# Performance work log

Hardware: AMD Instinct MI355X
Metric: run time of the kernel (lower is better)

The kernel has to match this reference:

```python
import jax, jax.numpy as jnp
import numpy as np

EPS = 1e-5


def gcn_conv(x, edge_index, W, b):
    # PyG GCNConv: h = x @ W; add self-loops; symmetric deg^-1/2 normalization; scatter-add to dst; + bias
    n = x.shape[0]
    h = x @ W  # [N, out]
    loops = jnp.arange(n, dtype=edge_index.dtype)
    src = jnp.concatenate([edge_index[0], loops])
    dst = jnp.concatenate([edge_index[1], loops])
    deg = jax.ops.segment_sum(jnp.ones(src.shape[0], dtype=h.dtype), dst, num_segments=n)
    dinv = jnp.where(deg > 0, jax.lax.rsqrt(jnp.maximum(deg, 1e-12)), 0.0)
    norm = dinv[src] * dinv[dst]  # [E+N]
    out = jax.ops.segment_sum(h[src] * norm[:, None], dst, num_segments=n)
    return out + b


def setup_inputs() -> dict:
    key = jax.random.key(0)
    ks = jax.random.split(key, 10)
    N, E = 50000, 800000
    IN, HID, OUT = 128, 128, 64
    x = jax.random.normal(ks[0], (N, IN), dtype=jnp.float32)
    edge_index1 = jax.random.randint(ks[1], (2, E), 0, N, dtype=jnp.int64)
    edge_index2 = jax.random.randint(ks[2], (2, E), 0, N, dtype=jnp.int64)
    s1 = 1.0 / np.sqrt(IN)
    s2 = 1.0 / np.sqrt(HID)
    W1 = jax.random.uniform(ks[3], (IN, HID), jnp.float32, -s1, s1)
    b1 = jax.random.uniform(ks[4], (HID,), jnp.float32, -s1, s1)
    gamma = jnp.ones((HID,), jnp.float32)
    beta = jnp.zeros((HID,), jnp.float32)
    W2 = jax.random.uniform(ks[5], (HID, OUT), jnp.float32, -s2, s2)
    b2 = jax.random.uniform(ks[6], (OUT,), jnp.float32, -s2, s2)
    return {"x": x, "edge_index1": edge_index1, "edge_index2": edge_index2,
            "W1": W1, "b1": b1, "gamma": gamma, "beta": beta, "W2": W2, "b2": b2}


def reference(x, edge_index1, edge_index2, W1, b1, gamma, beta, W2, b2):
    # layer 1: GCNConv -> (save hidden) -> BatchNorm1d (batch stats) -> ReLU -> dropout (identity, deterministic)
    h = gcn_conv(x, edge_index1, W1, b1)
    hidden = h
    mean = jnp.mean(h, axis=0)
    var = jnp.mean((h - mean) ** 2, axis=0)  # biased var, as torch BN uses for normalization
    h = (h - mean) * jax.lax.rsqrt(var + EPS) * gamma + beta
    h = jax.nn.relu(h)
    # layer 2: GCNConv (no norm/act on last layer)
    out = gcn_conv(h, edge_index2, W2, b2)
    return (out, hidden)
```

## Files before the change

### kernel.cpp

```cpp
#include <hip/hip_runtime.h>

#define GN 50000
#define GE 800000
#define HID 128
#define OUTC 64
#define NBK 196
#define NW  196
#define EPW 4096
#define PCAP 5888
#define A1B 2048

#define OFF_H1    0
#define OFF_H2    3200000
#define OFF_DINV1 4800000
#define OFF_DINV2 4850000
#define OFF_ROW1  4900000
#define OFF_ROW2  4950004
#define OFF_HIST  5000008
#define OFF_TOT   5076840
#define OFF_BBASE 5077232
#define OFF_BN    5077632
#define OFF_PART  5078144
#define OFF_PARTA 5602432
#define OFF_SRC1  5606528
#define OFF_SRC2  6406528
#define OFF_WT1   7206528
#define OFF_WT2   7214720

typedef __attribute__((ext_vector_type(8))) short bf16x8;
typedef __attribute__((ext_vector_type(4))) float f32x4;

__device__ inline unsigned bf16rne(float f) {
  unsigned u = __float_as_uint(f);
  return (u + 0x7FFFu + ((u >> 16) & 1u)) >> 16;
}
__device__ inline unsigned pack2(float a, float b) {
  return bf16rne(a) | (bf16rne(b) << 16);
}
__device__ inline float bflo(unsigned w) { return __uint_as_float(w << 16); }
__device__ inline float bfhi(unsigned w) { return __uint_as_float(w & 0xFFFF0000u); }
__device__ inline float bfs(unsigned short w) { return __uint_as_float(((unsigned)w) << 16); }

__global__ __launch_bounds__(256) void p1hist_kernel(const int* __restrict__ e1,
    const int* __restrict__ e2, int* __restrict__ hist) {
  __shared__ int h[NBK];
  int g = blockIdx.y, w = blockIdx.x;
  const int* dst = (g ? e2 : e1) + GE;
  for (int i = threadIdx.x; i < NBK; i += 256) h[i] = 0;
  __syncthreads();
  int i0 = w * EPW, iend = i0 + EPW; if (iend > GE) iend = GE;
  for (int i = i0 + threadIdx.x; i < iend; i += 256)
    atomicAdd(&h[dst[i] >> 8], 1);
  __syncthreads();
  int* out = hist + ((size_t)g * NW + w) * NBK;
  for (int i = threadIdx.x; i < NBK; i += 256) out[i] = h[i];
}

__global__ __launch_bounds__(256) void histscanA_kernel(int* __restrict__ hist,
    int* __restrict__ tot) {
  __shared__ int lds[256];
  int b = blockIdx.x, g = blockIdx.y, t = threadIdx.x;
  int* col = hist + (size_t)g * NW * NBK + b;
  int v = (t < NW) ? col[(size_t)t * NBK] : 0;
  lds[t] = v;
  __syncthreads();
  for (int off = 1; off < 256; off <<= 1) {
    int u = (t >= off) ? lds[t - off] : 0;
    __syncthreads();
    lds[t] += u;
    __syncthreads();
  }
  if (t < NW) col[(size_t)t * NBK] = lds[t] - v;
  if (t == NW - 1) tot[g * NBK + b] = lds[t];
}

__global__ __launch_bounds__(256) void histscanB_kernel(const int* __restrict__ tot,
    int* __restrict__ bbase) {
  __shared__ int lds[256];
  int t = threadIdx.x;
  for (int g = 0; g < 2; ++g) {
    int v = (t < NBK) ? tot[g * NBK + t] : 0;
    int orig = v;
    lds[t] = v;
    __syncthreads();
    for (int off = 1; off < 256; off <<= 1) {
      int u = (t >= off) ? lds[t - off] : 0;
      __syncthreads();
      lds[t] += u;
      __syncthreads();
    }
    if (t < NBK) bbase[g * (NBK + 1) + t] = lds[t] - orig;
    if (t == NBK - 1) bbase[g * (NBK + 1) + NBK] = lds[t];
    __syncthreads();
  }
}

__global__ __launch_bounds__(256) void p1scat_kernel(const int* __restrict__ e1,
    const int* __restrict__ e2, const int* __restrict__ hist,
    const int* __restrict__ bbase, int* __restrict__ pb1, int* __restrict__ pb2) {
  __shared__ int off[NBK];
  int g = blockIdx.y, w = blockIdx.x;
  const int* e = g ? e2 : e1;
  int* pb = g ? pb2 : pb1;
  const int* hrow = hist + ((size_t)g * NW + w) * NBK;
  const int* bb = bbase + g * (NBK + 1);
  for (int i = threadIdx.x; i < NBK; i += 256) off[i] = bb[i] + hrow[i];
  __syncthreads();
  int i0 = w * EPW, iend = i0 + EPW; if (iend > GE) iend = GE;
  for (int i = i0 + threadIdx.x; i < iend; i += 256) {
    int d = e[GE + i], s = e[i];
    int p = atomicAdd(&off[d >> 8], 1);
    pb[p] = s | ((d & 255) << 16);
  }
}

__global__ __launch_bounds__(256) void p2sort_kernel(const int* __restrict__ pb1,
    const int* __restrict__ pb2, const int* __restrict__ bbase,
    int* __restrict__ row1, int* __restrict__ row2,
    float* __restrict__ dinv1, float* __restrict__ dinv2,
    int* __restrict__ src1, int* __restrict__ src2) {
  __shared__ int stage[PCAP];
  __shared__ int lcnt[256], lc2[256], arr[256];
  __shared__ int lrow[257];
  int g = blockIdx.y, b = blockIdx.x, t = threadIdx.x;
  const int* pb = g ? pb2 : pb1;
  const int* bb = bbase + g * (NBK + 1);
  int* row = g ? row2 : row1;
  float* dinv = g ? dinv2 : dinv1;
  int* src = g ? src2 : src1;
  int lo = b << 8, hi = lo + 256; if (hi > GN) hi = GN;
  int nn = hi - lo;
  int base = bb[b], end = bb[b + 1], L = end - base;
  lcnt[t] = 0; lc2[t] = 0;
  __syncthreads();
  for (int i = base + t; i < end; i += 256)
    atomicAdd(&lcnt[((unsigned)pb[i]) >> 16], 1);
  __syncthreads();
  int v = lcnt[t];
  arr[t] = v;
  __syncthreads();
  for (int off = 1; off < 256; off <<= 1) {
    int u = (t >= off) ? arr[t - off] : 0;
    __syncthreads();
    arr[t] += u;
    __syncthreads();
  }
  lrow[t] = arr[t] - v;
  if (t == 255) lrow[256] = arr[255];
  __syncthreads();
  if (t < nn) {
    row[lo + t] = base + lrow[t];
    dinv[lo + t] = rsqrtf(1.0f + (float)lcnt[t]);
  }
  if (b == NBK - 1 && t == 0) row[GN] = end;
  if (L <= PCAP) {
    for (int i = base + t; i < end; i += 256) {
      unsigned p = (unsigned)pb[i];
      int ld = p >> 16;
      int rk = atomicAdd(&lc2[ld], 1);
      stage[lrow[ld] + rk] = (int)(p & 0xFFFFu);
    }
    __syncthreads();
    for (int i = t; i < L; i += 256) src[base + i] = stage[i];
  } else {
    for (int i = base + t; i < end; i += 256) {
      unsigned p = (unsigned)pb[i];
      int ld = p >> 16;
      int rk = atomicAdd(&lc2[ld], 1);
      src[base + lrow[ld] + rk] = (int)(p & 0xFFFFu);
    }
  }
}

__global__ __launch_bounds__(256) void wcvt_kernel(const float* __restrict__ W1,
    const float* __restrict__ W2, unsigned* __restrict__ wt1, unsigned* __restrict__ wt2) {
  int t = blockIdx.x * 256 + threadIdx.x;
  if (t < 8192) {
    int n = t >> 6, k2 = t & 63;
    wt1[t] = pack2(W1[(2 * k2) * 128 + n], W1[(2 * k2 + 1) * 128 + n]);
  }
  if (t < 4096) {
    int n = t >> 6, k2 = t & 63;
    wt2[t] = pack2(W2[(2 * k2) * 64 + n], W2[(2 * k2 + 1) * 64 + n]);
  }
}

__global__ __launch_bounds__(256) void gemm1_kernel(const float* __restrict__ A,
    const unsigned* __restrict__ wt1, const float* __restrict__ dinv1,
    unsigned short* __restrict__ h1u) {
  __shared__ unsigned a_lds[64 * 68];
  __shared__ unsigned w_lds[128 * 68];
  int t = threadIdx.x;
  int row0 = blockIdx.x * 64;
  for (int i = t; i < 128 * 64; i += 256)
    w_lds[(i >> 6) * 68 + (i & 63)] = wt1[i];
  for (int i = t; i < 64 * 32; i += 256) {
    int m = i >> 5, k4 = i & 31;
    int gr = row0 + m;
    float4 v = (gr < GN) ? ((const float4*)A)[(size_t)gr * 32 + k4]
                         : make_float4(0.f, 0.f, 0.f, 0.f);
    unsigned* dst = &a_lds[m * 68 + k4 * 2];
    dst[0] = pack2(v.x, v.y);
    dst[1] = pack2(v.z, v.w);
  }
  __syncthreads();
  int lane = t & 63, w = t >> 6;
  int n16 = lane & 15, quad = lane >> 4;
  int mbase = (w & 1) * 32;
  int nbase = (w >> 1) * 64;
  f32x4 acc[2][4] = {};
  const unsigned short* als = (const unsigned short*)a_lds;
  const unsigned short* wls = (const unsigned short*)w_lds;
  #pragma unroll
  for (int ks = 0; ks < 4; ++ks) {
    int k0 = ks * 32 + quad * 8;
    bf16x8 a0 = *(const bf16x8*)(als + (mbase + n16) * 136 + k0);
    bf16x8 a1 = *(const bf16x8*)(als + (mbase + 16 + n16) * 136 + k0);
    #pragma unroll
    for (int nt = 0; nt < 4; ++nt) {
      bf16x8 bf = *(const bf16x8*)(wls + (nbase + nt * 16 + n16) * 136 + k0);
      acc[0][nt] = __builtin_amdgcn_mfma_f32_16x16x32_bf16(a0, bf, acc[0][nt], 0, 0, 0);
      acc[1][nt] = __builtin_amdgcn_mfma_f32_16x16x32_bf16(a1, bf, acc[1][nt], 0, 0, 0);
    }
  }
  #pragma unroll
  for (int mt = 0; mt < 2; ++mt) {
    #pragma unroll
    for (int r = 0; r < 4; ++r) {
      int row_g = row0 + mbase + mt * 16 + quad * 4 + r;
      if (row_g < GN) {
        float dv = dinv1[row_g];
        #pragma unroll
        for (int nt = 0; nt < 4; ++nt) {
          int col = nbase + nt * 16 + n16;
          h1u[(size_t)row_g * 128 + col] = (unsigned short)bf16rne(dv * acc[mt][nt][r]);
        }
      }
    }
  }
}

__global__ __launch_bounds__(256) void gemm2_kernel(const float* __restrict__ A,
    const unsigned* __restrict__ wt2, const float* __restrict__ scale,
    const float* __restrict__ shift, const float* __restrict__ dinv2,
    unsigned short* __restrict__ h2u) {
  __shared__ unsigned a_lds[64 * 68];
  __shared__ unsigned w_lds[64 * 68];
  __shared__ float sc[128], sh[128];
  int t = threadIdx.x;
  if (t < 128) { sc[t] = scale[t]; sh[t] = shift[t]; }
  int row0 = blockIdx.x * 64;
  for (int i = t; i < 64 * 64; i += 256)
    w_lds[(i >> 6) * 68 + (i & 63)] = wt2[i];
  __syncthreads();
  for (int i = t; i < 64 * 32; i += 256) {
    int m = i >> 5, k4 = i & 31;
    int gr = row0 + m;
    float4 v = (gr < GN) ? ((const float4*)A)[(size_t)gr * 32 + k4]
                         : make_float4(0.f, 0.f, 0.f, 0.f);
    int c = k4 * 4;
    v.x = fmaxf(fmaf(v.x, sc[c],     sh[c]),     0.f);
    v.y = fmaxf(fmaf(v.y, sc[c + 1], sh[c + 1]), 0.f);
    v.z = fmaxf(fmaf(v.z, sc[c + 2], sh[c + 2]), 0.f);
    v.w = fmaxf(fmaf(v.w, sc[c + 3], sh[c + 3]), 0.f);
    unsigned* dst = &a_lds[m * 68 + k4 * 2];
    dst[0] = pack2(v.x, v.y);
    dst[1] = pack2(v.z, v.w);
  }
  __syncthreads();
  int lane = t & 63, w = t >> 6;
  int n16 = lane & 15, quad = lane >> 4;
  f32x4 acc[4] = {};
  const unsigned short* als = (const unsigned short*)a_lds;
  const unsigned short* wls = (const unsigned short*)w_lds;
  #pragma unroll
  for (int ks = 0; ks < 4; ++ks) {
    int k0 = ks * 32 + quad * 8;
    bf16x8 af = *(const bf16x8*)(als + (w * 16 + n16) * 136 + k0);
    #pragma unroll
    for (int nt = 0; nt < 4; ++nt) {
      bf16x8 bf = *(const bf16x8*)(wls + (nt * 16 + n16) * 136 + k0);
      acc[nt] = __builtin_amdgcn_mfma_f32_16x16x32_bf16(af, bf, acc[nt], 0, 0, 0);
    }
  }
  #pragma unroll
  for (int r = 0; r < 4; ++r) {
    int row_g = row0 + w * 16 + quad * 4 + r;
    if (row_g < GN) {
      float dv = dinv2[row_g];
      #pragma unroll
      for (int nt = 0; nt < 4; ++nt) {
        int col = nt * 16 + n16;
        h2u[(size_t)row_g * 64 + col] = (unsigned short)bf16rne(dv * acc[nt][r]);
      }
    }
  }
}

__global__ __launch_bounds__(256) void agg1_kernel(const unsigned* __restrict__ h1b,
    const int* __restrict__ row, const int* __restrict__ srcs,
    const float* __restrict__ dinv, const float* __restrict__ b1,
    float* __restrict__ hidden, float* __restrict__ part) {
  __shared__ float ps[256];
  int t = threadIdx.x;
  int lane = t & 63;
  float2 b = ((const float2*)b1)[lane];
  float sx = 0.f, sy = 0.f, qx = 0.f, qy = 0.f;
  int wid = (blockIdx.x * 256 + t) >> 6;
  for (int d = wid; d < GN; d += A1B * 4) {
    float di = dinv[d];
    unsigned sw = h1b[(size_t)d * 64 + lane];
    float ax = bflo(sw), ay = bfhi(sw);
    int e0 = row[d], e1 = row[d + 1];
    int i = e0;
    while ((i & 3) && i < e1) {
      unsigned v = h1b[(size_t)srcs[i] * 64 + lane];
      ax += bflo(v); ay += bfhi(v);
      ++i;
    }
    for (; i + 8 <= e1; i += 8) {
      int4 sa = *(const int4*)&srcs[i];
      int4 sb = *(const int4*)&srcs[i + 4];
      unsigned v0 = h1b[(size_t)sa.x * 64 + lane], v1 = h1b[(size_t)sa.y * 64 + lane];
      unsigned v2 = h1b[(size_t)sa.z * 64 + lane], v3 = h1b[(size_t)sa.w * 64 + lane];
      unsigned v4 = h1b[(size_t)sb.x * 64 + lane], v5 = h1b[(size_t)sb.y * 64 + lane];
      unsigned v6 = h1b[(size_t)sb.z * 64 + lane], v7 = h1b[(size_t)sb.w * 64 + lane];
      ax += bflo(v0); ay += bfhi(v0);
      ax += bflo(v1); ay += bfhi(v1);
      ax += bflo(v2); ay += bfhi(v2);
      ax += bflo(v3); ay += bfhi(v3);
      ax += bflo(v4); ay += bfhi(v4);
      ax += bflo(v5); ay += bfhi(v5);
      ax += bflo(v6); ay += bfhi(v6);
      ax += bflo(v7); ay += bfhi(v7);
    }
    if (i + 4 <= e1) {
      int4 sa = *(const int4*)&srcs[i];
      unsigned v0 = h1b[(size_t)sa.x * 64 + lane], v1 = h1b[(size_t)sa.y * 64 + lane];
      unsigned v2 = h1b[(size_t)sa.z * 64 + lane], v3 = h1b[(size_t)sa.w * 64 + lane];
      ax += bflo(v0); ay += bfhi(v0);
      ax += bflo(v1); ay += bfhi(v1);
      ax += bflo(v2); ay += bfhi(v2);
      ax += bflo(v3); ay += bfhi(v3);
      i += 4;
    }
    for (; i < e1; ++i) {
      unsigned v = h1b[(size_t)srcs[i] * 64 + lane];
      ax += bflo(v); ay += bfhi(v);
    }
    float ox = ax * di + b.x, oy = ay * di + b.y;
    float2 o; o.x = ox; o.y = oy;
    ((float2*)(hidden + (size_t)d * 128))[lane] = o;
    sx += ox; sy += oy; qx += ox * ox; qy += oy * oy;
  }
  float* pout = part + (size_t)blockIdx.x * 256;
  ps[t] = sx; __syncthreads();
  if (t < 64) pout[2 * t] = ps[t] + ps[t + 64] + ps[t + 128] + ps[t + 192];
  __syncthreads();
  ps[t] = sy; __syncthreads();
  if (t < 64) pout[2 * t + 1] = ps[t] + ps[t + 64] + ps[t + 128] + ps[t + 192];
  __syncthreads();
  ps[t] = qx; __syncthreads();
  if (t < 64) pout[128 + 2 * t] = ps[t] + ps[t + 64] + ps[t + 128] + ps[t + 192];
  __syncthreads();
  ps[t] = qy; __syncthreads();
  if (t < 64) pout[128 + 2 * t + 1] = ps[t] + ps[t + 64] + ps[t + 128] + ps[t + 192];
}

__global__ __launch_bounds__(256) void bn_reduceA_kernel(const float* __restrict__ part,
    float* __restrict__ partA) {
  int r = blockIdx.x, t = threadIdx.x;
  float s = 0.f;
  for (int k = 0; k < A1B / 16; ++k)
    s += part[((size_t)r * (A1B / 16) + k) * 256 + t];
  partA[r * 256 + t] = s;
}

__global__ __launch_bounds__(128) void bn_final_kernel(const float* __restrict__ partA,
    const float* __restrict__ gamma, const float* __restrict__ beta,
    float* __restrict__ scale, float* __restrict__ shift) {
  int c = threadIdx.x;
  float S = 0.f, Q = 0.f;
  for (int r = 0; r < 16; ++r) {
    S += partA[r * 256 + c];
    Q += partA[r * 256 + 128 + c];
  }
  float mean = S * (1.0f / GN);
  float var = Q * (1.0f / GN) - mean * mean;
  float istd = rsqrtf(var + 1e-5f);
  float g = gamma[c] * istd;
  scale[c] = g;
  shift[c] = beta[c] - mean * g;
}

__global__ __launch_bounds__(256) void agg2_kernel(const unsigned short* __restrict__ h2b,
    const int* __restrict__ row, const int* __restrict__ srcs,
    const float* __restrict__ dinv, const float* __restrict__ b2,
    float* __restrict__ out) {
  int wave = (blockIdx.x * 256 + threadIdx.x) >> 6;
  int lane = threadIdx.x & 63;
  if (wave >= GN) return;
  int d = wave;
  float di = dinv[d];
  float acc = bfs(h2b[(size_t)d * 64 + lane]);
  int e0 = row[d], e1 = row[d + 1];
  int i = e0;
  while ((i & 3) && i < e1) {
    acc += bfs(h2b[(size_t)srcs[i] * 64 + lane]);
    ++i;
  }
  for (; i + 8 <= e1; i += 8) {
    int4 sa = *(const int4*)&srcs[i];
    int4 sb = *(const int4*)&srcs[i + 4];
    float v0 = bfs(h2b[(size_t)sa.x * 64 + lane]), v1 = bfs(h2b[(size_t)sa.y * 64 + lane]);
    float v2 = bfs(h2b[(size_t)sa.z * 64 + lane]), v3 = bfs(h2b[(size_t)sa.w * 64 + lane]);
    float v4 = bfs(h2b[(size_t)sb.x * 64 + lane]), v5 = bfs(h2b[(size_t)sb.y * 64 + lane]);
    float v6 = bfs(h2b[(size_t)sb.z * 64 + lane]), v7 = bfs(h2b[(size_t)sb.w * 64 + lane]);
    acc += v0 + v1 + v2 + v3 + v4 + v5 + v6 + v7;
  }
  if (i + 4 <= e1) {
    int4 sa = *(const int4*)&srcs[i];
    acc += bfs(h2b[(size_t)sa.x * 64 + lane]) + bfs(h2b[(size_t)sa.y * 64 + lane])
         + bfs(h2b[(size_t)sa.z * 64 + lane]) + bfs(h2b[(size_t)sa.w * 64 + lane]);
    i += 4;
  }
  for (; i < e1; ++i)
    acc += bfs(h2b[(size_t)srcs[i] * 64 + lane]);
  out[(size_t)d * 64 + lane] = acc * di + b2[lane];
}

extern "C" void kernel_launch(void* const* d_in, const int* in_sizes, int n_in,
                              void* d_out, int out_size, void* d_ws, size_t ws_size,
                              hipStream_t stream) {
  const float* x     = (const float*)d_in[0];
  const int*   e1    = (const int*)d_in[1];
  const int*   e2    = (const int*)d_in[2];
  const float* W1    = (const float*)d_in[3];
  const float* b1    = (const float*)d_in[4];
  const float* gamma = (const float*)d_in[5];
  const float* beta  = (const float*)d_in[6];
  const float* W2    = (const float*)d_in[7];
  const float* b2    = (const float*)d_in[8];

  float* out    = (float*)d_out;
  float* hidden = out + (size_t)GN * OUTC;

  float*          ws    = (float*)d_ws;
  unsigned*       h1b   = (unsigned*)(ws + OFF_H1);
  unsigned*       h2b   = (unsigned*)(ws + OFF_H2);
  float*          dinv1 = ws + OFF_DINV1;
  float*          dinv2 = ws + OFF_DINV2;
  int*            row1  = (int*)(ws + OFF_ROW1);
  int*            row2  = (int*)(ws + OFF_ROW2);
  int*            hist  = (int*)(ws + OFF_HIST);
  int*            tot   = (int*)(ws + OFF_TOT);
  int*            bbase = (int*)(ws + OFF_BBASE);
  float*          bnbuf = ws + OFF_BN;
  float*          part  = ws + OFF_PART;
  float*          partA = ws + OFF_PARTA;
  int*            src1  = (int*)(ws + OFF_SRC1);
  int*            src2  = (int*)(ws + OFF_SRC2);
  unsigned*       wt1   = (unsigned*)(ws + OFF_WT1);
  unsigned*       wt2   = (unsigned*)(ws + OFF_WT2);
  int*            pb1   = (int*)h2b;
  int*            pb2   = pb1 + GE;

  wcvt_kernel<<<32, 256, 0, stream>>>(W1, W2, wt1, wt2);
  p1hist_kernel<<<dim3(NW, 2), 256, 0, stream>>>(e1, e2, hist);
  histscanA_kernel<<<dim3(NBK, 2), 256, 0, stream>>>(hist, tot);
  histscanB_kernel<<<1, 256, 0, stream>>>(tot, bbase);
  p1scat_kernel<<<dim3(NW, 2), 256, 0, stream>>>(e1, e2, hist, bbase, pb1, pb2);
  p2sort_kernel<<<dim3(NBK, 2), 256, 0, stream>>>(pb1, pb2, bbase,
                                                  row1, row2, dinv1, dinv2, src1, src2);

  gemm1_kernel<<<(GN + 63) / 64, 256, 0, stream>>>(x, wt1, dinv1,
                                                   (unsigned short*)h1b);
  agg1_kernel<<<A1B, 256, 0, stream>>>(h1b, row1, src1, dinv1, b1, hidden, part);

  bn_reduceA_kernel<<<16, 256, 0, stream>>>(part, partA);
  bn_final_kernel<<<1, 128, 0, stream>>>(partA, gamma, beta, bnbuf, bnbuf + 128);

  gemm2_kernel<<<(GN + 63) / 64, 256, 0, stream>>>(hidden, wt2, bnbuf, bnbuf + 128,
                                                   dinv2, (unsigned short*)h2b);
  agg2_kernel<<<(GN * 64 + 255) / 256, 256, 0, stream>>>(
      (const unsigned short*)h2b, row2, src2, dinv2, b2, out);
}
```

Baseline: 229.7 us.

## Fuse weight conversion and BN reduction, split gathers across half-waves

Removes the separate weight-conversion kernel by packing W1/W2 to bf16 directly inside each GEMM block's LDS load. The two-stage BN partial reduction is replaced with block-level atomicAdd into a small accumulator, zeroed in the histogram kernel, which drops two launches. The aggregation kernels now have each half-wave gather alternate edges with wider per-lane loads and combine the halves with a cross-lane shuffle. The aim is to cut launch overhead and raise memory-level parallelism in the gathers. In exchange, every GEMM block redoes the weight conversion with strided reads, and float atomics make the BN sums order-nondeterministic.

```diff
diff --git a/kernel.cpp b/kernel.cpp
--- a/kernel.cpp
+++ b/kernel.cpp
@@ -39,12 +39,12 @@
 }
 __device__ inline float bflo(unsigned w) { return __uint_as_float(w << 16); }
 __device__ inline float bfhi(unsigned w) { return __uint_as_float(w & 0xFFFF0000u); }
-__device__ inline float bfs(unsigned short w) { return __uint_as_float(((unsigned)w) << 16); }
 
 __global__ __launch_bounds__(256) void p1hist_kernel(const int* __restrict__ e1,
-    const int* __restrict__ e2, int* __restrict__ hist) {
+    const int* __restrict__ e2, int* __restrict__ hist, float* __restrict__ bnacc) {
   __shared__ int h[NBK];
   int g = blockIdx.y, w = blockIdx.x;
+  if (g == 0 && w == 0) bnacc[threadIdx.x] = 0.f;
   const int* dst = (g ? e2 : e1) + GE;
   for (int i = threadIdx.x; i < NBK; i += 256) h[i] = 0;
   __syncthreads();
@@ -172,28 +172,17 @@
   }
 }
 
-__global__ __launch_bounds__(256) void wcvt_kernel(const float* __restrict__ W1,
-    const float* __restrict__ W2, unsigned* __restrict__ wt1, unsigned* __restrict__ wt2) {
-  int t = blockIdx.x * 256 + threadIdx.x;
-  if (t < 8192) {
-    int n = t >> 6, k2 = t & 63;
-    wt1[t] = pack2(W1[(2 * k2) * 128 + n], W1[(2 * k2 + 1) * 128 + n]);
-  }
-  if (t < 4096) {
-    int n = t >> 6, k2 = t & 63;
-    wt2[t] = pack2(W2[(2 * k2) * 64 + n], W2[(2 * k2 + 1) * 64 + n]);
-  }
-}
-
 __global__ __launch_bounds__(256) void gemm1_kernel(const float* __restrict__ A,
-    const unsigned* __restrict__ wt1, const float* __restrict__ dinv1,
+    const float* __restrict__ W1, const float* __restrict__ dinv1,
     unsigned short* __restrict__ h1u) {
   __shared__ unsigned a_lds[64 * 68];
   __shared__ unsigned w_lds[128 * 68];
   int t = threadIdx.x;
   int row0 = blockIdx.x * 64;
-  for (int i = t; i < 128 * 64; i += 256)
-    w_lds[(i >> 6) * 68 + (i & 63)] = wt1[i];
+  for (int i = t; i < 128 * 64; i += 256) {
+    int k2 = i >> 7, n = i & 127;
+    w_lds[n * 68 + k2] = pack2(W1[(2 * k2) * 128 + n], W1[(2 * k2 + 1) * 128 + n]);
+  }
   for (int i = t; i < 64 * 32; i += 256) {
     int m = i >> 5, k4 = i & 31;
     int gr = row0 + m;
@@ -241,7 +230,7 @@
 }
 
 __global__ __launch_bounds__(256) void gemm2_kernel(const float* __restrict__ A,
-    const unsigned* __restrict__ wt2, const float* __restrict__ scale,
+    const float* __restrict__ W2, const float* __restrict__ scale,
     const float* __restrict__ shift, const float* __restrict__ dinv2,
     unsigned short* __restrict__ h2u) {
   __shared__ unsigned a_lds[64 * 68];
@@ -250,8 +239,10 @@
   int t = threadIdx.x;
   if (t < 128) { sc[t] = scale[t]; sh[t] = shift[t]; }
   int row0 = blockIdx.x * 64;
-  for (int i = t; i < 64 * 64; i += 256)
-    w_lds[(i >> 6) * 68 + (i & 63)] = wt2[i];
+  for (int i = t; i < 64 * 64; i += 256) {
+    int k2 = i >> 6, n = i & 63;
+    w_lds[n * 68 + k2] = pack2(W2[(2 * k2) * 64 + n], W2[(2 * k2 + 1) * 64 + n]);
+  }
   __syncthreads();
   for (int i = t; i < 64 * 32; i += 256) {
     int m = i >> 5, k4 = i & 31;
@@ -300,91 +291,94 @@
 __global__ __launch_bounds__(256) void agg1_kernel(const unsigned* __restrict__ h1b,
     const int* __restrict__ row, const int* __restrict__ srcs,
     const float* __restrict__ dinv, const float* __restrict__ b1,
-    float* __restrict__ hidden, float* __restrict__ part) {
-  __shared__ float ps[256];
+    float* __restrict__ hidden, float* __restrict__ bnacc) {
+  __shared__ float ps[4][128];
   int t = threadIdx.x;
-  int lane = t & 63;
-  float2 b = ((const float2*)b1)[lane];
-  float sx = 0.f, sy = 0.f, qx = 0.f, qy = 0.f;
+  int lane = t & 63, w = t >> 6;
+  int half = lane >> 5, l32 = lane & 31;
+  float4 bias = ((const float4*)b1)[l32];
+  float s0 = 0, s1 = 0, s2 = 0, s3 = 0, q0 = 0, q1 = 0, q2 = 0, q3 = 0;
   int wid = (blockIdx.x * 256 + t) >> 6;
   for (int d = wid; d < GN; d += A1B * 4) {
     float di = dinv[d];
-    unsigned sw = h1b[(size_t)d * 64 + lane];
-    float ax = bflo(sw), ay = bfhi(sw);
+    float a0 = 0, a1 = 0, a2 = 0, a3 = 0;
+    if (half) {
+      uint2 sv = ((const uint2*)(h1b + (size_t)d * 64))[l32];
+      a0 = bflo(sv.x); a1 = bfhi(sv.x); a2 = bflo(sv.y); a3 = bfhi(sv.y);
+    }
     int e0 = row[d], e1 = row[d + 1];
-    int i = e0;
+    int i = e0, j = 0;
     while ((i & 3) && i < e1) {
-      unsigned v = h1b[(size_t)srcs[i] * 64 + lane];
-      ax += bflo(v); ay += bfhi(v);
-      ++i;
+      if ((j & 1) == half) {
+        uint2 v = ((const uint2*)(h1b + (size_t)srcs[i] * 64))[l32];
+        a0 += bflo(v.x); a1 += bfhi(v.x); a2 += bflo(v.y); a3 += bfhi(v.y);
+      }
+      ++i; ++j;
     }
     for (; i + 8 <= e1; i += 8) {
       int4 sa = *(const int4*)&srcs[i];
       int4 sb = *(const int4*)&srcs[i + 4];
-      unsigned v0 = h1b[(size_t)sa.x * 64 + lane], v1 = h1b[(size_t)sa.y * 64 + lane];
-      unsigned v2 = h1b[(size_t)sa.z * 64 + lane], v3 = h1b[(size_t)sa.w * 64 + lane];
-      unsigned v4 = h1b[(size_t)sb.x * 64 + lane], v5 = h1b[(size_t)sb.y * 64 + lane];
-      unsigned v6 = h1b[(size_t)sb.z * 64 + lane], v7 = h1b[(size_t)sb.w * 64 + lane];
-      ax += bflo(v0); ay += bfhi(v0);
-      ax += bflo(v1); ay += bfhi(v1);
-      ax += bflo(v2); ay += bfhi(v2);
-      ax += bflo(v3); ay += bfhi(v3);
-      ax += bflo(v4); ay += bfhi(v4);
-      ax += bflo(v5); ay += bfhi(v5);
-      ax += bflo(v6); ay += bfhi(v6);
-      ax += bflo(v7); ay += bfhi(v7);
+      int sA = half ? sa.y : sa.x;
+      int sB = half ? sa.w : sa.z;
+      int sC = half ? sb.y : sb.x;
+      int sD = half ? sb.w : sb.z;
+      uint2 v0 = ((const uint2*)(h1b + (size_t)sA * 64))[l32];
+      uint2 v1 = ((const uint2*)(h1b + (size_t)sB * 64))[l32];
+      uint2 v2 = ((const uint2*)(h1b + (size_t)sC * 64))[l32];
+      uint2 v3 = ((const uint2*)(h1b + (size_t)sD * 64))[l32];
+      a0 += bflo(v0.x); a1 += bfhi(v0.x); a2 += bflo(v0.y); a3 += bfhi(v0.y);
+      a0 += bflo(v1.x); a1 += bfhi(v1.x); a2 += bflo(v1.y); a3 += bfhi(v1.y);
+      a0 += bflo(v2.x); a1 += bfhi(v2.x); a2 += bflo(v2.y); a3 += bfhi(v2.y);
+      a0 += bflo(v3.x); a1 += bfhi(v3.x); a2 += bflo(v3.y); a3 += bfhi(v3.y);
     }
     if (i + 4 <= e1) {
       int4 sa = *(const int4*)&srcs[i];
-      unsigned v0 = h1b[(size_t)sa.x * 64 + lane], v1 = h1b[(size_t)sa.y * 64 + lane];
-      unsigned v2 = h1b[(size_t)sa.z * 64 + lane], v3 = h1b[(size_t)sa.w * 64 + lane];
-      ax += bflo(v0); ay += bfhi(v0);
-      ax += bflo(v1); ay += bfhi(v1);
-      ax += bflo(v2); ay += bfhi(v2);
-      ax += bflo(v3); ay += bfhi(v3);
+      int sA = half ? sa.y : sa.x;
+      int sB = half ? sa.w : sa.z;
+      uint2 v0 = ((const uint2*)(h1b + (size_t)sA * 64))[l32];
+      uint2 v1 = ((const uint2*)(h1b + (size_t)sB * 64))[l32];
+      a0 += bflo(v0.x); a1 += bfhi(v0.x); a2 += bflo(v0.y); a3 += bfhi(v0.y);
+      a0 += bflo(v1.x); a1 += bfhi(v1.x); a2 += bflo(v1.y); a3 += bfhi(v1.y);
       i += 4;
     }
-    for (; i < e1; ++i) {
-      unsigned v = h1b[(size_t)srcs[i] * 64 + lane];
-      ax += bflo(v); ay += bfhi(v);
-    }
-    float ox = ax * di + b.x, oy = ay * di + b.y;
-    float2 o; o.x = ox; o.y = oy;
-    ((float2*)(hidden + (size_t)d * 128))[lane] = o;
-    sx += ox; sy += oy; qx += ox * ox; qy += oy * oy;
-  }
-  float* pout = part + (size_t)blockIdx.x * 256;
-  ps[t] = sx; __syncthreads();
-  if (t < 64) pout[2 * t] = ps[t] + ps[t + 64] + ps[t + 128] + ps[t + 192];
-  __syncthreads();
-  ps[t] = sy; __syncthreads();
-  if (t < 64) pout[2 * t + 1] = ps[t] + ps[t + 64] + ps[t + 128] + ps[t + 192];
-  __syncthreads();
-  ps[t] = qx; __syncthreads();
-  if (t < 64) pout[128 + 2 * t] = ps[t] + ps[t + 64] + ps[t + 128] + ps[t + 192];
-  __syncthreads();
-  ps[t] = qy; __syncthreads();
-  if (t < 64) pout[128 + 2 * t + 1] = ps[t] + ps[t + 64] + ps[t + 128] + ps[t + 192];
-}
-
-__global__ __launch_bounds__(256) void bn_reduceA_kernel(const float* __restrict__ part,
-    float* __restrict__ partA) {
-  int r = blockIdx.x, t = threadIdx.x;
-  float s = 0.f;
-  for (int k = 0; k < A1B / 16; ++k)
-    s += part[((size_t)r * (A1B / 16) + k) * 256 + t];
-  partA[r * 256 + t] = s;
-}
-
-__global__ __launch_bounds__(128) void bn_final_kernel(const float* __restrict__ partA,
+    for (j = 0; i < e1; ++i, ++j) {
+      if ((j & 1) == half) {
+        uint2 v = ((const uint2*)(h1b + (size_t)srcs[i] * 64))[l32];
+        a0 += bflo(v.x); a1 += bfhi(v.x); a2 += bflo(v.y); a3 += bfhi(v.y);
+      }
+    }
+    a0 += __shfl_xor(a0, 32, 64);
+    a1 += __shfl_xor(a1, 32, 64);
+    a2 += __shfl_xor(a2, 32, 64);
+    a3 += __shfl_xor(a3, 32, 64);
+    if (!half) {
+      float o0 = fmaf(a0, di, bias.x), o1 = fmaf(a1, di, bias.y);
+      float o2 = fmaf(a2, di, bias.z), o3 = fmaf(a3, di, bias.w);
+      ((float4*)(hidden + (size_t)d * 128))[l32] = make_float4(o0, o1, o2, o3);
+      s0 += o0; s1 += o1; s2 += o2; s3 += o3;
+      q0 += o0 * o0; q1 += o1 * o1; q2 += o2 * o2; q3 += o3 * o3;
+    }
+  }
+  if (!half) {
+    float* pw = &ps[w][0];
+    pw[4 * l32] = s0; pw[4 * l32 + 1] = s1; pw[4 * l32 + 2] = s2; pw[4 * l32 + 3] = s3;
+  }
+  __syncthreads();
+  if (t < 128) atomicAdd(&bnacc[t], ps[0][t] + ps[1][t] + ps[2][t] + ps[3][t]);
+  __syncthreads();
+  if (!half) {
+    float* pw = &ps[w][0];
+    pw[4 * l32] = q0; pw[4 * l32 + 1] = q1; pw[4 * l32 + 2] = q2; pw[4 * l32 + 3] = q3;
+  }
+  __syncthreads();
+  if (t < 128) atomicAdd(&bnacc[128 + t], ps[0][t] + ps[1][t] + ps[2][t] + ps[3][t]);
+}
+
+__global__ __launch_bounds__(128) void bn_final_kernel(const float* __restrict__ bnacc,
     const float* __restrict__ gamma, const float* __restrict__ beta,
     float* __restrict__ scale, float* __restrict__ shift) {
   int c = threadIdx.x;
-  float S = 0.f, Q = 0.f;
-  for (int r = 0; r < 16; ++r) {
-    S += partA[r * 256 + c];
-    Q += partA[r * 256 + 128 + c];
-  }
+  float S = bnacc[c], Q = bnacc[128 + c];
   float mean = S * (1.0f / GN);
   float var = Q * (1.0f / GN) - mean * mean;
   float istd = rsqrtf(var + 1e-5f);
@@ -393,40 +387,70 @@
   shift[c] = beta[c] - mean * g;
 }
 
-__global__ __launch_bounds__(256) void agg2_kernel(const unsigned short* __restrict__ h2b,
+__global__ __launch_bounds__(256) void agg2_kernel(const unsigned* __restrict__ h2b,
     const int* __restrict__ row, const int* __restrict__ srcs,
     const float* __restrict__ dinv, const float* __restrict__ b2,
     float* __restrict__ out) {
-  int wave = (blockIdx.x * 256 + threadIdx.x) >> 6;
+  int d = (blockIdx.x * 256 + threadIdx.x) >> 6;
   int lane = threadIdx.x & 63;
-  if (wave >= GN) return;
-  int d = wave;
+  int half = lane >> 5, l32 = lane & 31;
+  if (d >= GN) return;
   float di = dinv[d];
-  float acc = bfs(h2b[(size_t)d * 64 + lane]);
+  float a0 = 0, a1 = 0;
+  if (half) {
+    unsigned sv = h2b[(size_t)d * 32 + l32];
+    a0 = bflo(sv); a1 = bfhi(sv);
+  }
   int e0 = row[d], e1 = row[d + 1];
-  int i = e0;
+  int i = e0, j = 0;
   while ((i & 3) && i < e1) {
-    acc += bfs(h2b[(size_t)srcs[i] * 64 + lane]);
-    ++i;
+    if ((j & 1) == half) {
+      unsigned v = h2b[(size_t)srcs[i] * 32 + l32];
+      a0 += bflo(v); a1 += bfhi(v);
+    }
+    ++i; ++j;
   }
   for (; i + 8 <= e1; i += 8) {
     int4 sa = *(const int4*)&srcs[i];
     int4 sb = *(const int4*)&srcs[i + 4];
-    float v0 = bfs(h2b[(size_t)sa.x * 64 + lane]), v1 = bfs(h2b[(size_t)sa.y * 64 + lane]);
-    float v2 = bfs(h2b[(size_t)sa.z * 64 + lane]), v3 = bfs(h2b[(size_t)sa.w * 64 + lane]);
-    float v4 = bfs(h2b[(size_t)sb.x * 64 + lane]), v5 = bfs(h2b[(size_t)sb.y * 64 + lane]);
-    float v6 = bfs(h2b[(size_t)sb.z * 64 + lane]), v7 = bfs(h2b[(size_t)sb.w * 64 + lane]);
-    acc += v0 + v1 + v2 + v3 + v4 + v5 + v6 + v7;
+    int sA = half ? sa.y : sa.x;
+    int sB = half ? sa.w : sa.z;
+    int sC = half ? sb.y : sb.x;
+    int sD = half ? sb.w : sb.z;
+    unsigned v0 = h2b[(size_t)sA * 32 + l32];
+    unsigned v1 = h2b[(size_t)sB * 32 + l32];
+    unsigned v2 = h2b[(size_t)sC * 32 + l32];
+    unsigned v3 = h2b[(size_t)sD * 32 + l32];
+    a0 += bflo(v0); a1 += bfhi(v0);
+    a0 += bflo(v1); a1 += bfhi(v1);
+    a0 += bflo(v2); a1 += bfhi(v2);
+    a0 += bflo(v3); a1 += bfhi(v3);
   }
   if (i + 4 <= e1) {
     int4 sa = *(const int4*)&srcs[i];
-    acc += bfs(h2b[(size_t)sa.x * 64 + lane]) + bfs(h2b[(size_t)sa.y * 64 + lane])
-         + bfs(h2b[(size_t)sa.z * 64 + lane]) + bfs(h2b[(size_t)sa.w * 64 + lane]);
+    int sA = half ? sa.y : sa.x;
+    int sB = half ? sa.w : sa.z;
+    unsigned v0 = h2b[(size_t)sA * 32 + l32];
+    unsigned v1 = h2b[(size_t)sB * 32 + l32];
+    a0 += bflo(v0); a1 += bfhi(v0);
+    a0 += bflo(v1); a1 += bfhi(v1);
     i += 4;
   }
-  for (; i < e1; ++i)
-    acc += bfs(h2b[(size_t)srcs[i] * 64 + lane]);
-  out[(size_t)d * 64 + lane] = acc * di + b2[lane];
+  for (j = 0; i < e1; ++i, ++j) {
+    if ((j & 1) == half) {
+      unsigned v = h2b[(size_t)srcs[i] * 32 + l32];
+      a0 += bflo(v); a1 += bfhi(v);
+    }
+  }
+  a0 += __shfl_xor(a0, 32, 64);
+  a1 += __shfl_xor(a1, 32, 64);
+  if (!half) {
+    float2 b = ((const float2*)b2)[l32];
+    float2 o;
+    o.x = fmaf(a0, di, b.x);
+    o.y = fmaf(a1, di, b.y);
+    ((float2*)(out + (size_t)d * 64))[l32] = o;
+  }
 }
 
 extern "C" void kernel_launch(void* const* d_in, const int* in_sizes, int n_in,
@@ -456,32 +480,27 @@
   int*            tot   = (int*)(ws + OFF_TOT);
   int*            bbase = (int*)(ws + OFF_BBASE);
   float*          bnbuf = ws + OFF_BN;
-  float*          part  = ws + OFF_PART;
-  float*          partA = ws + OFF_PARTA;
+  float*          bnacc = ws + OFF_PARTA;
   int*            src1  = (int*)(ws + OFF_SRC1);
   int*            src2  = (int*)(ws + OFF_SRC2);
-  unsigned*       wt1   = (unsigned*)(ws + OFF_WT1);
-  unsigned*       wt2   = (unsigned*)(ws + OFF_WT2);
   int*            pb1   = (int*)h2b;
   int*            pb2   = pb1 + GE;
 
-  wcvt_kernel<<<32, 256, 0, stream>>>(W1, W2, wt1, wt2);
-  p1hist_kernel<<<dim3(NW, 2), 256, 0, stream>>>(e1, e2, hist);
+  p1hist_kernel<<<dim3(NW, 2), 256, 0, stream>>>(e1, e2, hist, bnacc);
   histscanA_kernel<<<dim3(NBK, 2), 256, 0, stream>>>(hist, tot);
   histscanB_kernel<<<1, 256, 0, stream>>>(tot, bbase);
   p1scat_kernel<<<dim3(NW, 2), 256, 0, stream>>>(e1, e2, hist, bbase, pb1, pb2);
   p2sort_kernel<<<dim3(NBK, 2), 256, 0, stream>>>(pb1, pb2, bbase,
                                                   row1, row2, dinv1, dinv2, src1, src2);
 
-  gemm1_kernel<<<(GN + 63) / 64, 256, 0, stream>>>(x, wt1, dinv1,
+  gemm1_kernel<<<(GN + 63) / 64, 256, 0, stream>>>(x, W1, dinv1,
                                                    (unsigned short*)h1b);
-  agg1_kernel<<<A1B, 256, 0, stream>>>(h1b, row1, src1, dinv1, b1, hidden, part);
-
-  bn_reduceA_kernel<<<16, 256, 0, stream>>>(part, partA);
-  bn_final_kernel<<<1, 128, 0, stream>>>(partA, gamma, beta, bnbuf, bnbuf + 128);
-
-  gemm2_kernel<<<(GN + 63) / 64, 256, 0, stream>>>(hidden, wt2, bnbuf, bnbuf + 128,
+  agg1_kernel<<<A1B, 256, 0, stream>>>(h1b, row1, src1, dinv1, b1, hidden, bnacc);
+
+  bn_final_kernel<<<1, 128, 0, stream>>>(bnacc, gamma, beta, bnbuf, bnbuf + 128);
+
+  gemm2_kernel<<<(GN + 63) / 64, 256, 0, stream>>>(hidden, W2, bnbuf, bnbuf + 128,
                                                    dinv2, (unsigned short*)h2b);
   agg2_kernel<<<(GN * 64 + 255) / 256, 256, 0, stream>>>(
-      (const unsigned short*)h2b, row2, src2, dinv2, b2, out);
-}
+      h2b, row2, src2, dinv2, b2, out);
+}
```

Result: slower. 272.8 us (+18.8%).
